# Optimization experiments

Hardware: AMD Instinct MI355X
Metric: run time of the kernel (lower is better)

The kernel has to match this reference:

```python
import jax, jax.numpy as jnp
import numpy as np

D_IN = 128
D_OUT = 128
B, N = 8, 2048
NEG = -9e15


def setup_inputs() -> dict:
    key = jax.random.key(0)
    ks = jax.random.split(key, 7)
    x = jax.random.normal(ks[0], (B, N, D_IN), dtype=jnp.float32)
    adj = jax.random.randint(ks[1], (B, N, N), 0, 2).astype(jnp.float32)
    s_in = 1.0 / np.sqrt(D_IN)
    s_out = 1.0 / np.sqrt(D_OUT)
    s_g = 1.0 / np.sqrt(2 * D_OUT)
    # torch.nn.Linear weights stored pre-transposed: [in, out]
    W_w = jax.random.uniform(ks[2], (D_IN, D_OUT), jnp.float32, -s_in, s_in)
    W_b = jax.random.uniform(ks[3], (D_OUT,), jnp.float32, -s_in, s_in)
    A_w = jax.random.uniform(ks[4], (D_OUT, D_OUT), jnp.float32, -s_out, s_out)
    gate_w = jax.random.uniform(ks[5], (2 * D_OUT, 1), jnp.float32, -s_g, s_g)
    gate_b = jax.random.uniform(ks[6], (1,), jnp.float32, -s_g, s_g)
    return {"x": x, "adj": adj, "W_w": W_w, "W_b": W_b, "A_w": A_w,
            "gate_w": gate_w, "gate_b": gate_b}


def reference(x, adj, W_w, W_b, A_w, gate_w, gate_b):
    h = x @ W_w + W_b                                  # [B,N,D]
    e = jnp.einsum('bnd,bmd->bnm', h @ A_w, h)          # [B,N,N]
    e = e + jnp.swapaxes(e, 1, 2)                       # symmetric
    att = jnp.where(adj > 0, e, NEG)
    att = jax.nn.softmax(att, axis=1)                   # NOTE: dim=1 as in torch code
    att = att * adj
    h_prime = jax.nn.relu(jnp.einsum('bnm,bmd->bnd', att, h))
    coeff = jax.nn.sigmoid(jnp.concatenate([x, h_prime], axis=-1) @ gate_w + gate_b)  # [B,N,1]
    return coeff * x + (1.0 - coeff) * h_prime
```

## Files before the change

### kernel.cpp

```cpp
#include <hip/hip_runtime.h>
#include <hip/hip_bf16.h>

#define B_ 8
#define N_ 2048
#define D_ 128

typedef __bf16 bf16_t;
typedef __bf16 v8bf __attribute__((ext_vector_type(8)));
typedef float  v4f  __attribute__((ext_vector_type(4)));

__global__ __launch_bounds__(256) void k_prep(
    const float* __restrict__ Ww, const float* __restrict__ Aw,
    bf16_t* __restrict__ WT, bf16_t* __restrict__ AT)
{
    int idx = blockIdx.x * 256 + threadIdx.x;
    int o = idx >> 7, i = idx & 127;
    WT[idx] = (bf16_t)Ww[i * D_ + o];
    AT[idx] = (bf16_t)Aw[i * D_ + o];
}

__global__ __launch_bounds__(512) void k_hg(
    const float* __restrict__ x, const float* __restrict__ Wb,
    const bf16_t* __restrict__ WT, const bf16_t* __restrict__ AT,
    bf16_t* __restrict__ hb, bf16_t* __restrict__ gb)
{
    int tid = threadIdx.x;
    int lane = tid & 63;
    int wave = tid >> 6;
    int q = lane >> 4;
    int c = lane & 15;
    int rg = wave & 1;
    int dh = wave >> 1;
    int row0 = blockIdx.x * 32;
    int nrow = row0 + rg * 16;

    __shared__ float hs[32][132];

    v8bf ax[4];
#pragma unroll
    for (int kc = 0; kc < 4; ++kc) {
        const float* src = x + (size_t)(nrow + c) * D_ + kc * 32 + q * 8;
        float4 f0 = *(const float4*)src;
        float4 f1 = *(const float4*)(src + 4);
        v8bf a;
        a[0]=(bf16_t)f0.x; a[1]=(bf16_t)f0.y; a[2]=(bf16_t)f0.z; a[3]=(bf16_t)f0.w;
        a[4]=(bf16_t)f1.x; a[5]=(bf16_t)f1.y; a[6]=(bf16_t)f1.z; a[7]=(bf16_t)f1.w;
        ax[kc] = a;
    }

#pragma unroll
    for (int t = 0; t < 2; ++t) {
        int ct = dh * 2 + t;
        float bias = Wb[ct * 16 + c];
        v4f acc = {bias, bias, bias, bias};
#pragma unroll
        for (int kc = 0; kc < 4; ++kc) {
            v8bf bw = *(const v8bf*)(WT + (size_t)(ct * 16 + c) * D_ + kc * 32 + q * 8);
            acc = __builtin_amdgcn_mfma_f32_16x16x32_bf16(ax[kc], bw, acc, 0, 0, 0);
        }
#pragma unroll
        for (int r = 0; r < 4; ++r) hs[rg * 16 + q * 4 + r][ct * 16 + c] = acc[r];
    }
    __syncthreads();

    v8bf ahf[4];
#pragma unroll
    for (int kc = 0; kc < 4; ++kc) {
        v4f p0 = *(const v4f*)&hs[rg * 16 + c][kc * 32 + q * 8];
        v4f p1 = *(const v4f*)&hs[rg * 16 + c][kc * 32 + q * 8 + 4];
        v8bf a;
#pragma unroll
        for (int j = 0; j < 4; ++j) { a[j] = (bf16_t)p0[j]; a[j+4] = (bf16_t)p1[j]; }
        ahf[kc] = a;
    }
    {
        int r2 = tid >> 4, s = tid & 15;
        v4f p0 = *(const v4f*)&hs[r2][s * 8];
        v4f p1 = *(const v4f*)&hs[r2][s * 8 + 4];
        v8bf hv;
#pragma unroll
        for (int j = 0; j < 4; ++j) { hv[j] = (bf16_t)p0[j]; hv[j+4] = (bf16_t)p1[j]; }
        *(v8bf*)(hb + (size_t)(row0 + r2) * D_ + s * 8) = hv;
    }

    v4f gacc[2];
#pragma unroll
    for (int t = 0; t < 2; ++t) {
        int ct = dh * 2 + t;
        v4f acc = {0.f, 0.f, 0.f, 0.f};
#pragma unroll
        for (int kc = 0; kc < 4; ++kc) {
            v8bf bw = *(const v8bf*)(AT + (size_t)(ct * 16 + c) * D_ + kc * 32 + q * 8);
            acc = __builtin_amdgcn_mfma_f32_16x16x32_bf16(ahf[kc], bw, acc, 0, 0, 0);
        }
        gacc[t] = acc;
    }
    __syncthreads();
#pragma unroll
    for (int t = 0; t < 2; ++t) {
        int ct = dh * 2 + t;
#pragma unroll
        for (int r = 0; r < 4; ++r) hs[rg * 16 + q * 4 + r][ct * 16 + c] = gacc[t][r];
    }
    __syncthreads();
    {
        int r2 = tid >> 4, s = tid & 15;
        v4f p0 = *(const v4f*)&hs[r2][s * 8];
        v4f p1 = *(const v4f*)&hs[r2][s * 8 + 4];
        v8bf gv;
#pragma unroll
        for (int j = 0; j < 4; ++j) { gv[j] = (bf16_t)p0[j]; gv[j+4] = (bf16_t)p1[j]; }
        *(v8bf*)(gb + (size_t)(row0 + r2) * D_ + s * 8) = gv;
    }
}

__global__ __launch_bounds__(256, 3) void k_att(
    const bf16_t* __restrict__ hb, const bf16_t* __restrict__ gb,
    const float* __restrict__ adj, float* __restrict__ colsum,
    bf16_t* __restrict__ Pt)
{
    int bid = blockIdx.x;
    int b = bid & 7;
    int rest = bid >> 3;
    int nblk = rest >> 3;
    int mgrp = rest & 7;
    int tid = threadIdx.x;
    int wave = tid >> 6;
    int lane = tid & 63;
    int q = lane >> 4;
    int c = lane & 15;
    int nbase = nblk * 64;
    int mwav = mgrp * 256 + wave * 64;
    const size_t hgoff = (size_t)b * N_ * D_;
    const float* adjb = adj + (size_t)b * N_ * N_;

    __shared__ __align__(16) bf16_t hs[64][136];
    __shared__ __align__(16) bf16_t gs[64][136];

    {
        int r = tid >> 2, seg = tid & 3;
        const bf16_t* hsrc = hb + hgoff + (size_t)(nbase + r) * D_ + seg * 32;
        const bf16_t* gsrc = gb + hgoff + (size_t)(nbase + r) * D_ + seg * 32;
#pragma unroll
        for (int v = 0; v < 4; ++v) {
            *(v8bf*)&hs[r][seg * 32 + v * 8] = *(const v8bf*)(hsrc + v * 8);
            *(v8bf*)&gs[r][seg * 32 + v * 8] = *(const v8bf*)(gsrc + v * 8);
        }
    }
    __syncthreads();

    v8bf bh[4], bg[4], bhn[4], bgn[4];
#pragma unroll
    for (int kc = 0; kc < 4; ++kc) {
        size_t off = hgoff + (size_t)(mwav + c) * D_ + kc * 32 + q * 8;
        bh[kc] = *(const v8bf*)(hb + off);
        bg[kc] = *(const v8bf*)(gb + off);
    }

    for (int t = 0; t < 4; ++t) {
        int mt = mwav + t * 16;
        float av[4][4];
#pragma unroll
        for (int sub = 0; sub < 4; ++sub)
#pragma unroll
            for (int r = 0; r < 4; ++r)
                av[sub][r] = adjb[(size_t)(nbase + sub * 16 + q * 4 + r) * N_ + mt + c];
        if (t < 3) {
#pragma unroll
            for (int kc = 0; kc < 4; ++kc) {
                size_t off = hgoff + (size_t)(mt + 16 + c) * D_ + kc * 32 + q * 8;
                bhn[kc] = *(const v8bf*)(hb + off);
                bgn[kc] = *(const v8bf*)(gb + off);
            }
        }
        v4f e[4];
#pragma unroll
        for (int sub = 0; sub < 4; ++sub) e[sub] = (v4f){0.f, 0.f, 0.f, 0.f};
#pragma unroll
        for (int kc = 0; kc < 4; ++kc)
#pragma unroll
            for (int sub = 0; sub < 4; ++sub) {
                v8bf ag = *(const v8bf*)&gs[sub * 16 + c][kc * 32 + q * 8];
                v8bf ah = *(const v8bf*)&hs[sub * 16 + c][kc * 32 + q * 8];
                e[sub] = __builtin_amdgcn_mfma_f32_16x16x32_bf16(ag, bh[kc], e[sub], 0, 0, 0);
                e[sub] = __builtin_amdgcn_mfma_f32_16x16x32_bf16(ah, bg[kc], e[sub], 0, 0, 0);
            }
        float cs = 0.f;
#pragma unroll
        for (int sub = 0; sub < 4; ++sub)
#pragma unroll
            for (int r = 0; r < 4; ++r) {
                float ex = __expf(e[sub][r]);
                float pv = (av[sub][r] > 0.f) ? ex : 0.f;
                cs += pv;
                Pt[((size_t)b * N_ + nbase + sub * 16 + q * 4 + r) * N_ + mt + c] = (bf16_t)pv;
            }
        cs += __shfl_xor(cs, 16);
        cs += __shfl_xor(cs, 32);
        if (lane < 16) atomicAdd(&colsum[b * N_ + mt + lane], cs);
#pragma unroll
        for (int kc = 0; kc < 4; ++kc) { bh[kc] = bhn[kc]; bg[kc] = bgn[kc]; }
    }
}

__global__ __launch_bounds__(256) void k_scaleT(
    const bf16_t* __restrict__ hb, const float* __restrict__ colsum,
    bf16_t* __restrict__ hbTs)
{
    int bid = blockIdx.x;
    int b = bid >> 6;
    int rem = bid & 63;
    int nblk = rem >> 1;
    int dblk = rem & 1;
    int tid = threadIdx.x;
    __shared__ bf16_t sm[64][72];
    __shared__ float sinv[64];
    int n0 = nblk * 64, d0 = dblk * 64;
    int r = tid >> 3, cg = tid & 7;
#pragma unroll
    for (int rr = 0; rr < 2; ++rr) {
        int row = r + rr * 32;
        *(v8bf*)&sm[row][cg * 8] =
            *(const v8bf*)(hb + (size_t)(b * N_ + n0 + row) * D_ + d0 + cg * 8);
    }
    if (tid < 64) {
        float s = colsum[b * N_ + n0 + tid];
        sinv[tid] = (s > 0.f) ? 1.f / s : 0.f;
    }
    __syncthreads();
#pragma unroll
    for (int rr = 0; rr < 2; ++rr) {
        int dr = r + rr * 32;
        v8bf v;
#pragma unroll
        for (int jj = 0; jj < 8; ++jj)
            v[jj] = (bf16_t)((float)sm[cg * 8 + jj][dr] * sinv[cg * 8 + jj]);
        *(v8bf*)(hbTs + (size_t)(b * D_ + d0 + dr) * N_ + n0 + cg * 8) = v;
    }
}

__global__ __launch_bounds__(512, 4) void k_out(
    const bf16_t* __restrict__ Pt, const bf16_t* __restrict__ hbTs,
    const float* __restrict__ x, const float* __restrict__ gw,
    const float* __restrict__ gbias, float* __restrict__ out)
{
    int bid = blockIdx.x;
    int b = bid & 7;
    int nblk = bid >> 3;
    int tid = threadIdx.x;
    int wave = tid >> 6;
    int lane = tid & 63;
    int q = lane >> 4;
    int c = lane & 15;
    int nbase = nblk * 32;
    int m0 = wave * 256;

    __shared__ float hp[32][132];

    const bf16_t* hTb = hbTs + (size_t)b * D_ * N_;
    const bf16_t* Pb  = Pt + (size_t)b * N_ * N_;

    v4f acc[2][8];
#pragma unroll
    for (int sub = 0; sub < 2; ++sub)
#pragma unroll
        for (int dt = 0; dt < 8; ++dt) acc[sub][dt] = (v4f){0.f, 0.f, 0.f, 0.f};

    for (int ch = 0; ch < 8; ++ch) {
        int mch = m0 + ch * 32;
        v8bf a[2];
#pragma unroll
        for (int sub = 0; sub < 2; ++sub)
            a[sub] = *(const v8bf*)(Pb + (size_t)(nbase + sub * 16 + c) * N_ + mch + q * 8);
        v8bf vt[8];
#pragma unroll
        for (int dt = 0; dt < 8; ++dt)
            vt[dt] = *(const v8bf*)(hTb + (size_t)(dt * 16 + c) * N_ + mch + q * 8);
#pragma unroll
        for (int dt = 0; dt < 8; ++dt)
#pragma unroll
            for (int sub = 0; sub < 2; ++sub)
                acc[sub][dt] = __builtin_amdgcn_mfma_f32_16x16x32_bf16(a[sub], vt[dt], acc[sub][dt], 0, 0, 0);
    }

    if (wave == 0) {
#pragma unroll
        for (int sub = 0; sub < 2; ++sub)
#pragma unroll
            for (int dt = 0; dt < 8; ++dt)
#pragma unroll
                for (int r = 0; r < 4; ++r)
                    hp[sub * 16 + q * 4 + r][dt * 16 + c] = acc[sub][dt][r];
    }
    __syncthreads();
#pragma unroll
    for (int wv = 1; wv < 8; ++wv) {
        if (wave == wv) {
#pragma unroll
            for (int sub = 0; sub < 2; ++sub)
#pragma unroll
                for (int dt = 0; dt < 8; ++dt)
#pragma unroll
                    for (int r = 0; r < 4; ++r)
                        hp[sub * 16 + q * 4 + r][dt * 16 + c] += acc[sub][dt][r];
        }
        __syncthreads();
    }

    int row = tid >> 4;
    int seg = tid & 15;
    size_t g = (size_t)b * N_ + nbase + row;
    const float* xr = x + g * D_ + seg * 8;
    float4 xa = *(const float4*)xr;
    float4 xb = *(const float4*)(xr + 4);
    float hv[8];
#pragma unroll
    for (int j = 0; j < 8; ++j) hv[j] = fmaxf(hp[row][seg * 8 + j], 0.f);
    float part = xa.x * gw[seg*8+0] + xa.y * gw[seg*8+1] + xa.z * gw[seg*8+2] + xa.w * gw[seg*8+3]
               + xb.x * gw[seg*8+4] + xb.y * gw[seg*8+5] + xb.z * gw[seg*8+6] + xb.w * gw[seg*8+7];
#pragma unroll
    for (int j = 0; j < 8; ++j) part += hv[j] * gw[D_ + seg * 8 + j];
    part += __shfl_xor(part, 1);
    part += __shfl_xor(part, 2);
    part += __shfl_xor(part, 4);
    part += __shfl_xor(part, 8);
    float coeff = 1.f / (1.f + __expf(-(part + gbias[0])));
    float4 o0, o1;
    o0.x = coeff * xa.x + (1.f - coeff) * hv[0];
    o0.y = coeff * xa.y + (1.f - coeff) * hv[1];
    o0.z = coeff * xa.z + (1.f - coeff) * hv[2];
    o0.w = coeff * xa.w + (1.f - coeff) * hv[3];
    o1.x = coeff * xb.x + (1.f - coeff) * hv[4];
    o1.y = coeff * xb.y + (1.f - coeff) * hv[5];
    o1.z = coeff * xb.z + (1.f - coeff) * hv[6];
    o1.w = coeff * xb.w + (1.f - coeff) * hv[7];
    float* orow = out + g * D_ + seg * 8;
    *(float4*)orow = o0;
    *(float4*)(orow + 4) = o1;
}

extern "C" void kernel_launch(void* const* d_in, const int* in_sizes, int n_in,
                              void* d_out, int out_size, void* d_ws, size_t ws_size,
                              hipStream_t stream)
{
    const float* x     = (const float*)d_in[0];
    const float* adj   = (const float*)d_in[1];
    const float* Ww    = (const float*)d_in[2];
    const float* Wb    = (const float*)d_in[3];
    const float* Aw    = (const float*)d_in[4];
    const float* gw    = (const float*)d_in[5];
    const float* gbias = (const float*)d_in[6];
    float* out = (float*)d_out;

    char* ws = (char*)d_ws;
    bf16_t* hb     = (bf16_t*)(ws);
    bf16_t* gb     = (bf16_t*)(ws + (4 << 20));
    bf16_t* hbTs   = (bf16_t*)(ws + (8 << 20));
    float*  colsum = (float*)(ws + (12 << 20));
    bf16_t* Pt     = (bf16_t*)(ws + (17 << 20));
    bf16_t* WT     = (bf16_t*)(ws + (81 << 20));
    bf16_t* AT     = (bf16_t*)(ws + (81 << 20) + (32 << 10));

    hipMemsetAsync(colsum, 0, B_ * N_ * sizeof(float), stream);
    k_prep<<<64, 256, 0, stream>>>(Ww, Aw, WT, AT);
    k_hg<<<B_ * N_ / 32, 512, 0, stream>>>(x, Wb, WT, AT, hb, gb);
    k_att<<<2048, 256, 0, stream>>>(hb, gb, adj, colsum, Pt);
    k_scaleT<<<512, 256, 0, stream>>>(hb, colsum, hbTs);
    k_out<<<512, 512, 0, stream>>>(Pt, hbTs, x, gw, gbias, out);
}
```

Baseline: 336.6 us.

## Stage exp tile in LDS for coalesced adj reads and Pt stores

The attention kernel now works on 32-row n-tiles instead of 64, doubling the grid, and raises the occupancy hint to 4. Each wave writes its exponentiated scores into a per-wave LDS buffer, then reads adj with float4 loads and writes Pt with 8-wide bf16 vector stores along rows. This replaces the scattered 16-element per-row accesses and accumulates column sums per lane before atomics. The cost is doubled h/g tile reloads, twice as many colsum atomics, extra LDS traffic, and reliance on a wave barrier for intra-wave LDS visibility.

```diff
diff --git a/kernel.cpp b/kernel.cpp
--- a/kernel.cpp
+++ b/kernel.cpp
@@ -114,7 +114,7 @@
     }
 }
 
-__global__ __launch_bounds__(256, 3) void k_att(
+__global__ __launch_bounds__(256, 4) void k_att(
     const bf16_t* __restrict__ hb, const bf16_t* __restrict__ gb,
     const float* __restrict__ adj, float* __restrict__ colsum,
     bf16_t* __restrict__ Pt)
@@ -129,22 +129,26 @@
     int lane = tid & 63;
     int q = lane >> 4;
     int c = lane & 15;
-    int nbase = nblk * 64;
+    int nbase = nblk * 32;
     int mwav = mgrp * 256 + wave * 64;
     const size_t hgoff = (size_t)b * N_ * D_;
     const float* adjb = adj + (size_t)b * N_ * N_;
 
-    __shared__ __align__(16) bf16_t hs[64][136];
-    __shared__ __align__(16) bf16_t gs[64][136];
+    __shared__ __align__(16) bf16_t hs[32][136];
+    __shared__ __align__(16) bf16_t gs[32][136];
+    __shared__ __align__(16) bf16_t eb_all[4][32][72];
+    bf16_t (*eb)[72] = eb_all[wave];
 
     {
-        int r = tid >> 2, seg = tid & 3;
-        const bf16_t* hsrc = hb + hgoff + (size_t)(nbase + r) * D_ + seg * 32;
-        const bf16_t* gsrc = gb + hgoff + (size_t)(nbase + r) * D_ + seg * 32;
-#pragma unroll
-        for (int v = 0; v < 4; ++v) {
-            *(v8bf*)&hs[r][seg * 32 + v * 8] = *(const v8bf*)(hsrc + v * 8);
-            *(v8bf*)&gs[r][seg * 32 + v * 8] = *(const v8bf*)(gsrc + v * 8);
+        int r = tid >> 3;
+        int ch0 = tid & 7;
+#pragma unroll
+        for (int cc = 0; cc < 2; ++cc) {
+            int ch = ch0 + cc * 8;
+            *(v8bf*)&hs[r][ch * 8] =
+                *(const v8bf*)(hb + hgoff + (size_t)(nbase + r) * D_ + ch * 8);
+            *(v8bf*)&gs[r][ch * 8] =
+                *(const v8bf*)(gb + hgoff + (size_t)(nbase + r) * D_ + ch * 8);
         }
     }
     __syncthreads();
@@ -158,48 +162,68 @@
     }
 
     for (int t = 0; t < 4; ++t) {
-        int mt = mwav + t * 16;
-        float av[4][4];
-#pragma unroll
-        for (int sub = 0; sub < 4; ++sub)
-#pragma unroll
-            for (int r = 0; r < 4; ++r)
-                av[sub][r] = adjb[(size_t)(nbase + sub * 16 + q * 4 + r) * N_ + mt + c];
         if (t < 3) {
+            int mt = mwav + (t + 1) * 16;
 #pragma unroll
             for (int kc = 0; kc < 4; ++kc) {
-                size_t off = hgoff + (size_t)(mt + 16 + c) * D_ + kc * 32 + q * 8;
+                size_t off = hgoff + (size_t)(mt + c) * D_ + kc * 32 + q * 8;
                 bhn[kc] = *(const v8bf*)(hb + off);
                 bgn[kc] = *(const v8bf*)(gb + off);
             }
         }
-        v4f e[4];
-#pragma unroll
-        for (int sub = 0; sub < 4; ++sub) e[sub] = (v4f){0.f, 0.f, 0.f, 0.f};
+        v4f e[2];
+        e[0] = (v4f){0.f, 0.f, 0.f, 0.f};
+        e[1] = (v4f){0.f, 0.f, 0.f, 0.f};
 #pragma unroll
         for (int kc = 0; kc < 4; ++kc)
 #pragma unroll
-            for (int sub = 0; sub < 4; ++sub) {
+            for (int sub = 0; sub < 2; ++sub) {
                 v8bf ag = *(const v8bf*)&gs[sub * 16 + c][kc * 32 + q * 8];
                 v8bf ah = *(const v8bf*)&hs[sub * 16 + c][kc * 32 + q * 8];
                 e[sub] = __builtin_amdgcn_mfma_f32_16x16x32_bf16(ag, bh[kc], e[sub], 0, 0, 0);
                 e[sub] = __builtin_amdgcn_mfma_f32_16x16x32_bf16(ah, bg[kc], e[sub], 0, 0, 0);
             }
-        float cs = 0.f;
-#pragma unroll
-        for (int sub = 0; sub < 4; ++sub)
-#pragma unroll
-            for (int r = 0; r < 4; ++r) {
-                float ex = __expf(e[sub][r]);
-                float pv = (av[sub][r] > 0.f) ? ex : 0.f;
-                cs += pv;
-                Pt[((size_t)b * N_ + nbase + sub * 16 + q * 4 + r) * N_ + mt + c] = (bf16_t)pv;
-            }
-        cs += __shfl_xor(cs, 16);
-        cs += __shfl_xor(cs, 32);
-        if (lane < 16) atomicAdd(&colsum[b * N_ + mt + lane], cs);
+#pragma unroll
+        for (int sub = 0; sub < 2; ++sub)
+#pragma unroll
+            for (int r = 0; r < 4; ++r)
+                eb[sub * 16 + q * 4 + r][t * 16 + c] = (bf16_t)__expf(e[sub][r]);
 #pragma unroll
         for (int kc = 0; kc < 4; ++kc) { bh[kc] = bhn[kc]; bg[kc] = bgn[kc]; }
+    }
+    __builtin_amdgcn_wave_barrier();
+
+    int prow = lane >> 3, pseg = lane & 7;
+    float cs[8];
+#pragma unroll
+    for (int j = 0; j < 8; ++j) cs[j] = 0.f;
+#pragma unroll
+    for (int pass = 0; pass < 4; ++pass) {
+        int row = pass * 8 + prow;
+        v8bf e8 = *(const v8bf*)&eb[row][pseg * 8];
+        const float* ap = adjb + (size_t)(nbase + row) * N_ + mwav + pseg * 8;
+        float4 a0 = *(const float4*)ap;
+        float4 a1 = *(const float4*)(ap + 4);
+        float am[8] = {a0.x, a0.y, a0.z, a0.w, a1.x, a1.y, a1.z, a1.w};
+        v8bf o;
+#pragma unroll
+        for (int j = 0; j < 8; ++j) {
+            bool live = am[j] > 0.f;
+            o[j] = live ? e8[j] : (bf16_t)0.f;
+            cs[j] += live ? (float)e8[j] : 0.f;
+        }
+        *(v8bf*)(Pt + ((size_t)b * N_ + nbase + row) * N_ + mwav + pseg * 8) = o;
+    }
+#pragma unroll
+    for (int j = 0; j < 8; ++j) {
+        cs[j] += __shfl_xor(cs[j], 8);
+        cs[j] += __shfl_xor(cs[j], 16);
+        cs[j] += __shfl_xor(cs[j], 32);
+    }
+    if (lane < 8) {
+#pragma unroll
+        for (int j = 0; j < 8; ++j)
+            atomicAdd(&colsum[b * N_ + mwav + lane * 8 + j], cs[j]);
     }
 }
 
@@ -364,7 +388,7 @@
     hipMemsetAsync(colsum, 0, B_ * N_ * sizeof(float), stream);
     k_prep<<<64, 256, 0, stream>>>(Ww, Aw, WT, AT);
     k_hg<<<B_ * N_ / 32, 512, 0, stream>>>(x, Wb, WT, AT, hb, gb);
-    k_att<<<2048, 256, 0, stream>>>(hb, gb, adj, colsum, Pt);
+    k_att<<<4096, 256, 0, stream>>>(hb, gb, adj, colsum, Pt);
     k_scaleT<<<512, 256, 0, stream>>>(hb, colsum, hbTs);
     k_out<<<512, 512, 0, stream>>>(Pt, hbTs, x, gw, gbias, out);
 }
```

Measured after the change: 329.7 us. 2.0% less time.
